# Kernel tuning notes

Hardware: AMD Instinct MI355X
Metric: run time of the kernel (lower is better)

The kernel has to match this reference:

```python
import jax, jax.numpy as jnp
import numpy as np

B, H, N, D = 1, 8, 2048, 64  # n >> d: fastmax's intended long-seq / small-head-dim regime


def setup_inputs() -> dict:
    key = jax.random.key(0)
    kq, kk, kv, kr = jax.random.split(key, 4)
    q = jax.random.normal(kq, (B, H, N, D), dtype=jnp.float32)
    k = jax.random.normal(kk, (B, H, N, D), dtype=jnp.float32)
    v = jax.random.normal(kv, (B, H, N, D), dtype=jnp.float32)
    rpe_matrix = jax.random.normal(kr, (2 * N - 1, D), dtype=jnp.float32)
    return {"q": q, "k": k, "v": v, "rpe_matrix": rpe_matrix, "mask": 1}


def reference(q, k, v, rpe_matrix, mask):
    # Fastmax: 2nd-order Taylor approximation of softmax attention,
    # weight(i,j) = 1 + s_ij + s_ij^2 / 2 where s_ij = q_i . (k_j) + q_i . rpe[i-j+n-1],
    # normalized by the row-sum, optionally causal (mask).
    b, h, n, d = q.shape
    # content scores: (b,h,n,n)
    s = jnp.einsum('bhid,bhjd->bhij', q, k)
    # RPE scores: project q onto every relative-position embedding, then gather
    # the (i,j) -> i-j+n-1 diagonal structure.  qr: (b,h,n,2n-1)
    qr = jnp.einsum('bhid,md->bhim', q, rpe_matrix)
    i = jnp.arange(n)[:, None]
    j = jnp.arange(n)[None, :]
    rel = i - j + (n - 1)  # (n,n) in [0, 2n-2]
    s = s + jnp.take_along_axis(qr, rel[None, None], axis=-1)
    # Taylor-2 exp approximation
    w = 1.0 + s + 0.5 * s * s
    if mask:  # causal
        w = jnp.where(j <= i, w, 0.0)
    denom = jnp.sum(w, axis=-1, keepdims=True)  # (b,h,n,1)
    out = jnp.einsum('bhij,bhjd->bhid', w, v) / denom
    return out
```

## Files before the change

### kernel.cpp

```cpp
#include <hip/hip_runtime.h>
#include <hip/hip_bf16.h>

#define HH 8
#define NN 2048
#define DD 64

typedef __attribute__((ext_vector_type(8))) short bf16x8;
typedef __attribute__((ext_vector_type(4))) float f32x4;
typedef __attribute__((ext_vector_type(8))) unsigned short u16x8;
typedef unsigned short ushort_t;

static __device__ __forceinline__ unsigned short f2bf(float x) {
    union { float f; unsigned u; } un; un.f = x;
    unsigned r = un.u + 0x7FFFu + ((un.u >> 16) & 1u);
    return (unsigned short)(r >> 16);
}
static __device__ __forceinline__ float bf2f(unsigned short u) {
    union { unsigned u; float f; } un; un.u = ((unsigned)u) << 16;
    return un.f;
}

#define OFF_Q  0u
#define OFF_K  2097152u
#define OFF_VT 4194304u
#define OFF_R  6291456u
#define OFF_P  6815744u
#define WS_NEED 11272192u

#define NQ4 262144
#define NR4 65520
#define CVT_BLOCKS 2305
__global__ void pre_kernel(const float* __restrict__ q, const float* __restrict__ k,
                           const float* __restrict__ r, const float* __restrict__ v,
                           ushort_t* __restrict__ ws) {
    __shared__ __align__(16) ushort_t T[64][72];
    if (blockIdx.x < CVT_BLOCKS) {
        int idx = blockIdx.x * 256 + threadIdx.x;
        const float* src; ushort_t* dst; int off;
        if (idx < NQ4) { src = q; dst = (ushort_t*)((char*)ws + OFF_Q); off = idx; }
        else if (idx < 2 * NQ4) { src = k; dst = (ushort_t*)((char*)ws + OFF_K); off = idx - NQ4; }
        else if (idx < 2 * NQ4 + NR4) { src = r; dst = (ushort_t*)((char*)ws + OFF_R); off = idx - 2 * NQ4; }
        else return;
        float4 f = *(const float4*)&src[4 * (size_t)off];
        ushort4 u; u.x = f2bf(f.x); u.y = f2bf(f.y); u.z = f2bf(f.z); u.w = f2bf(f.w);
        *(ushort4*)&dst[4 * (size_t)off] = u;
    } else {
        ushort_t* vt = (ushort_t*)((char*)ws + OFF_VT);
        const int bb = blockIdx.x - CVT_BLOCKS;
        const int h = bb >> 5;
        const int n0 = (bb & 31) * 64;
        const int tid = threadIdx.x;
        const float* vh = v + (size_t)h * NN * DD;
        #pragma unroll
        for (int p = 0; p < 4; ++p) {
            int c = tid + 256 * p; int rr = c >> 4, dc = (c & 15) << 2;
            float4 f = *(const float4*)&vh[(size_t)(n0 + rr) * DD + dc];
            T[dc + 0][rr] = f2bf(f.x); T[dc + 1][rr] = f2bf(f.y);
            T[dc + 2][rr] = f2bf(f.z); T[dc + 3][rr] = f2bf(f.w);
        }
        __syncthreads();
        #pragma unroll
        for (int p = 0; p < 2; ++p) {
            int c = tid + 256 * p; int d = c >> 3, nn = (c & 7) << 3;
            *(u16x8*)&vt[((size_t)h * 64 + d) * NN + n0 + nn] = *(const u16x8*)&T[d][nn];
        }
    }
}

__global__ __launch_bounds__(256, 2)
void fastmax_main(const ushort_t* __restrict__ wsb, float* __restrict__ outg,
                  float* __restrict__ wsPart)
{
    __shared__ __align__(16) ushort_t Ks[64][72];
    __shared__ __align__(16) ushort_t Bs[96][72];
    __shared__ __align__(16) ushort_t Vts[64][72];
    __shared__ __align__(16) float    Ts[4][16][50];
    __shared__ __align__(16) ushort_t Ws[4][16][40];
    __shared__ __align__(16) float    Epi[32][68];

    const ushort_t* qb  = (const ushort_t*)((const char*)wsb + OFF_Q);
    const ushort_t* kb  = (const ushort_t*)((const char*)wsb + OFF_K);
    const ushort_t* vtb = (const ushort_t*)((const char*)wsb + OFF_VT);
    const ushort_t* rb  = (const ushort_t*)((const char*)wsb + OFF_R);

    const int tid = threadIdx.x;
    const int w   = tid >> 6;
    const int l   = tid & 63;
    const int lq  = l >> 4;
    const int ln  = l & 15;
    const int rt  = w & 1;
    const int ch  = w >> 1;

    const int sb     = blockIdx.x & 1;
    const int stream = blockIdx.x >> 1;
    const int head   = stream & 7;
    const int p      = stream >> 3;
    const int tileA  = 63 - p;
    const int njtA   = (tileA >> 1) + 1;
    const int tileB  = p;
    const int njtB   = (tileB >> 1) + 1;

    const ushort_t* qh  = qb  + (size_t)head * NN * DD;
    const ushort_t* kh  = kb  + (size_t)head * NN * DD;
    const ushort_t* vth = vtb + (size_t)head * DD * NN;
    float*          oh  = outg + (size_t)head * NN * DD;

    const int sw = 16 * rt - 32 * ch + 32;

    #pragma unroll 1
    for (int tsel = 0; tsel < 2; ++tsel) {
        if (tsel == 1 && sb == 0) break;
        const int tile = tsel ? tileB : tileA;
        const int jlo  = tsel ? 0 : (sb ? 17 : 0);
        const int jhi  = tsel ? njtB : (sb ? njtA : 17);
        const int i0   = tile * 32;

        bf16x8 qf0 = *(const bf16x8*)&qh[(size_t)(i0 + 16 * rt + ln) * DD +  0 + 8 * lq];
        bf16x8 qf1 = *(const bf16x8*)&qh[(size_t)(i0 + 16 * rt + ln) * DD + 32 + 8 * lq];

        f32x4 acc0 = {0,0,0,0}, acc1 = {0,0,0,0}, acc2 = {0,0,0,0}, acc3 = {0,0,0,0};
        float denv0 = 0.f, denv1 = 0.f, denv2 = 0.f, denv3 = 0.f;

        for (int jt = jlo; jt < jhi; ++jt) {
            const int j0 = jt * 64;
            __syncthreads();

            #pragma unroll
            for (int p2 = 0; p2 < 2; ++p2) {
                int c = tid + 256 * p2; int r = c >> 3, dc = (c & 7) << 3;
                *(u16x8*)&Ks[r][dc] = *(const u16x8*)&kh[(size_t)(j0 + r) * DD + dc];
            }
            const int relbase = i0 - j0 + 1984;
            #pragma unroll
            for (int p2 = 0; p2 < 3; ++p2) {
                int c = tid + 256 * p2; int r = c >> 3, dc = (c & 7) << 3;
                int row = relbase + r; if (row > 4094) row = 4094;
                *(u16x8*)&Bs[r][dc] = *(const u16x8*)&rb[(size_t)row * DD + dc];
            }
            #pragma unroll
            for (int p2 = 0; p2 < 2; ++p2) {
                int c = tid + 256 * p2; int d = c >> 3, nc = (c & 7) << 3;
                *(u16x8*)&Vts[d][nc] = *(const u16x8*)&vth[(size_t)d * NN + j0 + nc];
            }
            __syncthreads();

            f32x4 s0 = {0,0,0,0}, s1 = {0,0,0,0};
            {
                bf16x8 b00 = *(const bf16x8*)&Ks[32 * ch      + ln][ 0 + 8 * lq];
                bf16x8 b01 = *(const bf16x8*)&Ks[32 * ch      + ln][32 + 8 * lq];
                bf16x8 b10 = *(const bf16x8*)&Ks[32 * ch + 16 + ln][ 0 + 8 * lq];
                bf16x8 b11 = *(const bf16x8*)&Ks[32 * ch + 16 + ln][32 + 8 * lq];
                s0 = __builtin_amdgcn_mfma_f32_16x16x32_bf16(qf0, b00, s0, 0, 0, 0);
                s0 = __builtin_amdgcn_mfma_f32_16x16x32_bf16(qf1, b01, s0, 0, 0, 0);
                s1 = __builtin_amdgcn_mfma_f32_16x16x32_bf16(qf0, b10, s1, 0, 0, 0);
                s1 = __builtin_amdgcn_mfma_f32_16x16x32_bf16(qf1, b11, s1, 0, 0, 0);
            }

            #pragma unroll
            for (int bt = 0; bt < 3; ++bt) {
                f32x4 t = {0,0,0,0};
                bf16x8 b0 = *(const bf16x8*)&Bs[sw + 16 * bt + ln][ 0 + 8 * lq];
                bf16x8 b1 = *(const bf16x8*)&Bs[sw + 16 * bt + ln][32 + 8 * lq];
                t = __builtin_amdgcn_mfma_f32_16x16x32_bf16(qf0, b0, t, 0, 0, 0);
                t = __builtin_amdgcn_mfma_f32_16x16x32_bf16(qf1, b1, t, 0, 0, 0);
                #pragma unroll
                for (int e = 0; e < 4; ++e)
                    Ts[w][4 * lq + e][16 * bt + ln] = t[e];
            }

            #pragma unroll
            for (int ct = 0; ct < 2; ++ct) {
                f32x4 sv = ct ? s1 : s0;
                #pragma unroll
                for (int e = 0; e < 4; ++e) {
                    int rp = 4 * lq + e;
                    int cp = 16 * ct + ln;
                    int bw = rp - cp + 31;
                    float s = sv[e] + Ts[w][rp][bw];
                    float wv = 1.0f + s + 0.5f * s * s;
                    if (j0 + 32 * ch + cp > i0 + 16 * rt + rp) wv = 0.0f;
                    ushort_t wb = f2bf(wv);
                    Ws[w][rp][cp] = wb;
                    float wr = bf2f(wb);
                    if (e == 0) denv0 += wr; else if (e == 1) denv1 += wr;
                    else if (e == 2) denv2 += wr; else denv3 += wr;
                }
            }

            {
                bf16x8 af = *(const bf16x8*)&Ws[w][ln][8 * lq];
                bf16x8 b;
                b = *(const bf16x8*)&Vts[ 0 + ln][32 * ch + 8 * lq];
                acc0 = __builtin_amdgcn_mfma_f32_16x16x32_bf16(af, b, acc0, 0, 0, 0);
                b = *(const bf16x8*)&Vts[16 + ln][32 * ch + 8 * lq];
                acc1 = __builtin_amdgcn_mfma_f32_16x16x32_bf16(af, b, acc1, 0, 0, 0);
                b = *(const bf16x8*)&Vts[32 + ln][32 * ch + 8 * lq];
                acc2 = __builtin_amdgcn_mfma_f32_16x16x32_bf16(af, b, acc2, 0, 0, 0);
                b = *(const bf16x8*)&Vts[48 + ln][32 * ch + 8 * lq];
                acc3 = __builtin_amdgcn_mfma_f32_16x16x32_bf16(af, b, acc3, 0, 0, 0);
            }
        }

        #pragma unroll
        for (int off = 1; off <= 8; off <<= 1) {
            denv0 += __shfl_xor(denv0, off);
            denv1 += __shfl_xor(denv1, off);
            denv2 += __shfl_xor(denv2, off);
            denv3 += __shfl_xor(denv3, off);
        }

        __syncthreads();
        if (ch == 0) {
            #pragma unroll
            for (int e = 0; e < 4; ++e) {
                int r = 16 * rt + 4 * lq + e;
                f32x4 a = (e == 0) ? acc0 : acc0;
                (void)a;
                Epi[r][ 0 + ln] = acc0[e];
                Epi[r][16 + ln] = acc1[e];
                Epi[r][32 + ln] = acc2[e];
                Epi[r][48 + ln] = acc3[e];
            }
            if (ln == 0) {
                Epi[16 * rt + 4 * lq + 0][64] = denv0;
                Epi[16 * rt + 4 * lq + 1][64] = denv1;
                Epi[16 * rt + 4 * lq + 2][64] = denv2;
                Epi[16 * rt + 4 * lq + 3][64] = denv3;
            }
        }
        __syncthreads();
        if (ch == 1) {
            #pragma unroll
            for (int e = 0; e < 4; ++e) {
                int r = 16 * rt + 4 * lq + e;
                Epi[r][ 0 + ln] += acc0[e];
                Epi[r][16 + ln] += acc1[e];
                Epi[r][32 + ln] += acc2[e];
                Epi[r][48 + ln] += acc3[e];
            }
            if (ln == 0) {
                Epi[16 * rt + 4 * lq + 0][64] += denv0;
                Epi[16 * rt + 4 * lq + 1][64] += denv1;
                Epi[16 * rt + 4 * lq + 2][64] += denv2;
                Epi[16 * rt + 4 * lq + 3][64] += denv3;
            }
        }
        __syncthreads();
        if (tsel == 0) {
            float* dst = wsPart + ((size_t)(head * 32 + p) * 2 + sb) * (32 * 68);
            for (int idx = tid; idx < 32 * 68; idx += 256) dst[idx] = (&Epi[0][0])[idx];
        } else {
            #pragma unroll
            for (int e2 = 0; e2 < 8; ++e2) {
                int idx = tid + 256 * e2;
                int r = idx >> 6, d = idx & 63;
                oh[(size_t)(i0 + r) * DD + d] = Epi[r][d] / Epi[r][64];
            }
        }
    }
}

__global__ void combine_kernel(const float* __restrict__ wsPart, float* __restrict__ outg) {
    const int blk = blockIdx.x;
    const int head = blk >> 5;
    const int p = blk & 31;
    const int tileA = 63 - p;
    const float* p0 = wsPart + (size_t)blk * 2 * (32 * 68);
    const float* p1 = p0 + 32 * 68;
    float* oh = outg + (size_t)head * NN * DD;
    #pragma unroll
    for (int e2 = 0; e2 < 8; ++e2) {
        int idx = threadIdx.x + 256 * e2;
        int r = idx >> 6, d = idx & 63;
        float num = p0[r * 68 + d] + p1[r * 68 + d];
        float den = p0[r * 68 + 64] + p1[r * 68 + 64];
        oh[(size_t)(tileA * 32 + r) * DD + d] = num / den;
    }
}

__global__ __launch_bounds__(256, 2)
void fastmax_fallback(const float* __restrict__ qg0, const float* __restrict__ kg0,
                      const float* __restrict__ vg0, const float* __restrict__ rg,
                      float* __restrict__ outg)
{
    __shared__ __align__(16) ushort_t Qs[32][72];
    __shared__ __align__(16) ushort_t Ks2[64][72];
    __shared__ __align__(16) ushort_t Bs2[96][72];
    __shared__ __align__(16) ushort_t Vts2[96][72];
    __shared__ __align__(16) float    Tsf[32][97];
    __shared__ __align__(16) ushort_t Wsf[32][72];
    __shared__ float denomLds[32];

    const int tid = threadIdx.x;
    const int w = tid >> 6, l = tid & 63, lq = l >> 4, ln = l & 15;
    const int head = blockIdx.x & 7, ib = blockIdx.x >> 3;
    const int it = 63 - ib, i0 = it * 32, njt = (it >> 1) + 1;
    const float* qg = qg0 + (size_t)head * NN * DD;
    const float* kg = kg0 + (size_t)head * NN * DD;
    const float* vg = vg0 + (size_t)head * NN * DD;
    float* og = outg + (size_t)head * NN * DD;
    {
        #pragma unroll
        for (int p = 0; p < 2; ++p) {
            int c = tid + 256 * p; int r = c >> 4, dc = (c & 15) << 2;
            float4 f = *(const float4*)&qg[(size_t)(i0 + r) * DD + dc];
            ushort4 u; u.x = f2bf(f.x); u.y = f2bf(f.y); u.z = f2bf(f.z); u.w = f2bf(f.w);
            *(ushort4*)&Qs[r][dc] = u;
        }
        for (int idx = tid; idx < 32 * 72; idx += 256) {
            int rr = idx / 72, cc = idx - rr * 72;
            Vts2[64 + rr][cc] = (rr == 0) ? (ushort_t)0x3F80 : (ushort_t)0;
        }
    }
    f32x4 a0 = {0,0,0,0}, a1 = {0,0,0,0}, a2 = {0,0,0,0};
    const int pr = w & 1, rt = w & 1, cp = w >> 1;
    for (int jt = 0; jt < njt; ++jt) {
        const int j0 = jt * 64;
        __syncthreads();
        #pragma unroll
        for (int p = 0; p < 4; ++p) {
            int c = tid + 256 * p; int r = c >> 4, dc = (c & 15) << 2;
            float4 f = *(const float4*)&kg[(size_t)(j0 + r) * DD + dc];
            ushort4 u; u.x = f2bf(f.x); u.y = f2bf(f.y); u.z = f2bf(f.z); u.w = f2bf(f.w);
            *(ushort4*)&Ks2[r][dc] = u;
        }
        const int relbase = i0 - j0 + 1984;
        #pragma unroll
        for (int p = 0; p < 6; ++p) {
            int c = tid + 256 * p; int r = c >> 4, dc = (c & 15) << 2;
            int row = relbase + r; if (row > 4094) row = 4094;
            float4 f = *(const float4*)&rg[(size_t)row * DD + dc];
            ushort4 u; u.x = f2bf(f.x); u.y = f2bf(f.y); u.z = f2bf(f.z); u.w = f2bf(f.w);
            *(ushort4*)&Bs2[r][dc] = u;
        }
        #pragma unroll
        for (int p = 0; p < 4; ++p) {
            int c = tid + 256 * p; int r = c >> 4, dc = (c & 15) << 2;
            float4 f = *(const float4*)&vg[(size_t)(j0 + r) * DD + dc];
            Vts2[dc + 0][r] = f2bf(f.x); Vts2[dc + 1][r] = f2bf(f.y);
            Vts2[dc + 2][r] = f2bf(f.z); Vts2[dc + 3][r] = f2bf(f.w);
        }
        __syncthreads();
        f32x4 s0 = {0,0,0,0}, s1 = {0,0,0,0};
        #pragma unroll
        for (int ks = 0; ks < 2; ++ks) {
            bf16x8 a = *(const bf16x8*)&Qs[16 * rt + ln][32 * ks + 8 * lq];
            bf16x8 b0 = *(const bf16x8*)&Ks2[32 * cp + ln][32 * ks + 8 * lq];
            bf16x8 b1 = *(const bf16x8*)&Ks2[32 * cp + 16 + ln][32 * ks + 8 * lq];
            s0 = __builtin_amdgcn_mfma_f32_16x16x32_bf16(a, b0, s0, 0, 0, 0);
            s1 = __builtin_amdgcn_mfma_f32_16x16x32_bf16(a, b1, s1, 0, 0, 0);
        }
        #pragma unroll
        for (int kk = 0; kk < 3; ++kk) {
            int bt = (w >> 1) + 2 * kk;
            f32x4 t = {0,0,0,0};
            #pragma unroll
            for (int ks = 0; ks < 2; ++ks) {
                bf16x8 a = *(const bf16x8*)&Qs[16 * rt + ln][32 * ks + 8 * lq];
                bf16x8 b = *(const bf16x8*)&Bs2[16 * bt + ln][32 * ks + 8 * lq];
                t = __builtin_amdgcn_mfma_f32_16x16x32_bf16(a, b, t, 0, 0, 0);
            }
            #pragma unroll
            for (int e = 0; e < 4; ++e) Tsf[16 * rt + 4 * lq + e][16 * bt + ln] = t[e];
        }
        __syncthreads();
        #pragma unroll
        for (int ct2 = 0; ct2 < 2; ++ct2) {
            f32x4 sv = ct2 ? s1 : s0;
            int c_loc = 32 * cp + 16 * ct2 + ln, j = j0 + c_loc;
            #pragma unroll
            for (int e = 0; e < 4; ++e) {
                int r_loc = 16 * rt + 4 * lq + e, i = i0 + r_loc;
                float s = sv[e] + Tsf[r_loc][r_loc - c_loc + 63];
                float wv = 1.0f + s + 0.5f * s * s;
                if (j > i) wv = 0.0f;
                Wsf[r_loc][c_loc] = f2bf(wv);
            }
        }
        __syncthreads();
        {
            bf16x8 af0 = *(const bf16x8*)&Wsf[16 * pr + ln][ 0 + 8 * lq];
            bf16x8 af1 = *(const bf16x8*)&Wsf[16 * pr + ln][32 + 8 * lq];
            int pn0 = w >> 1; bf16x8 b;
            b = *(const bf16x8*)&Vts2[16 * (pn0 + 0) + ln][ 0 + 8 * lq];
            a0 = __builtin_amdgcn_mfma_f32_16x16x32_bf16(af0, b, a0, 0, 0, 0);
            b = *(const bf16x8*)&Vts2[16 * (pn0 + 0) + ln][32 + 8 * lq];
            a0 = __builtin_amdgcn_mfma_f32_16x16x32_bf16(af1, b, a0, 0, 0, 0);
            b = *(const bf16x8*)&Vts2[16 * (pn0 + 2) + ln][ 0 + 8 * lq];
            a1 = __builtin_amdgcn_mfma_f32_16x16x32_bf16(af0, b, a1, 0, 0, 0);
            b = *(const bf16x8*)&Vts2[16 * (pn0 + 2) + ln][32 + 8 * lq];
            a1 = __builtin_amdgcn_mfma_f32_16x16x32_bf16(af1, b, a1, 0, 0, 0);
            b = *(const bf16x8*)&Vts2[16 * (pn0 + 4) + ln][ 0 + 8 * lq];
            a2 = __builtin_amdgcn_mfma_f32_16x16x32_bf16(af0, b, a2, 0, 0, 0);
            b = *(const bf16x8*)&Vts2[16 * (pn0 + 4) + ln][32 + 8 * lq];
            a2 = __builtin_amdgcn_mfma_f32_16x16x32_bf16(af1, b, a2, 0, 0, 0);
        }
    }
    if (w < 2 && ln == 0) {
        #pragma unroll
        for (int e = 0; e < 4; ++e) denomLds[16 * pr + 4 * lq + e] = a2[e];
    }
    __syncthreads();
    #pragma unroll
    for (int k = 0; k < 2; ++k) {
        int pn = (w >> 1) + 2 * k;
        f32x4 acc = k ? a1 : a0;
        #pragma unroll
        for (int e = 0; e < 4; ++e) {
            int r_loc = 16 * pr + 4 * lq + e;
            og[(size_t)(i0 + r_loc) * DD + 16 * pn + ln] = acc[e] / denomLds[r_loc];
        }
    }
}

extern "C" void kernel_launch(void* const* d_in, const int* in_sizes, int n_in,
                              void* d_out, int out_size, void* d_ws, size_t ws_size,
                              hipStream_t stream) {
    const float* q   = (const float*)d_in[0];
    const float* k   = (const float*)d_in[1];
    const float* v   = (const float*)d_in[2];
    const float* rpe = (const float*)d_in[3];
    float* out = (float*)d_out;

    if (ws_size >= WS_NEED) {
        ushort_t* wsb = (ushort_t*)d_ws;
        float* wsPart = (float*)((char*)d_ws + OFF_P);
        hipLaunchKernelGGL(pre_kernel, dim3(CVT_BLOCKS + 256), dim3(256), 0, stream,
                           q, k, rpe, v, wsb);
        hipLaunchKernelGGL(fastmax_main, dim3(512), dim3(256), 0, stream,
                           wsb, out, wsPart);
        hipLaunchKernelGGL(combine_kernel, dim3(256), dim3(256), 0, stream, wsPart, out);
    } else {
        hipLaunchKernelGGL(fastmax_fallback, dim3(512), dim3(256), 0, stream,
                           q, k, v, rpe, out);
    }
}
```

Measured before the change: 106.1 us.

## Double-buffer K/RPE/V tiles with register prefetch and store RPE scores as bf16

The K, RPE-band and V^T tiles are now double-buffered in LDS. The next tile's global loads are issued into registers before the compute on the current tile, which lets one barrier per iteration be dropped and hides global latency behind the MFMAs. To pay for the extra LDS, the per-wave RPE score scratch is stored as bf16 and aliased with the epilogue buffer in a shared union. The bf16 scratch adds rounding to the RPE score term, and the larger register and LDS footprint may lower occupancy under the 256x2 launch bound.

```diff
diff --git a/kernel.cpp b/kernel.cpp
--- a/kernel.cpp
+++ b/kernel.cpp
@@ -71,17 +71,18 @@
 void fastmax_main(const ushort_t* __restrict__ wsb, float* __restrict__ outg,
                   float* __restrict__ wsPart)
 {
-    __shared__ __align__(16) ushort_t Ks[64][72];
-    __shared__ __align__(16) ushort_t Bs[96][72];
-    __shared__ __align__(16) ushort_t Vts[64][72];
-    __shared__ __align__(16) float    Ts[4][16][50];
-    __shared__ __align__(16) ushort_t Ws[4][16][40];
-    __shared__ __align__(16) float    Epi[32][68];
+    __shared__ __align__(16) ushort_t Ks[2][64][72];
+    __shared__ __align__(16) ushort_t Bs[2][96][72];
+    __shared__ __align__(16) ushort_t Vts[2][64][72];
+    __shared__ __align__(16) unsigned char U[11776];
+    ushort_t* TsP = (ushort_t*)U;
+    ushort_t* WsP = (ushort_t*)(U + 6656);
+    float*    Epi = (float*)U;
 
     const ushort_t* qb  = (const ushort_t*)((const char*)wsb + OFF_Q);
     const ushort_t* kb  = (const ushort_t*)((const char*)wsb + OFF_K);
     const ushort_t* vtb = (const ushort_t*)((const char*)wsb + OFF_VT);
-    const ushort_t* rb  = (const ushort_t*)((const char*)wsb + OFF_R);
+    const ushort_t* rb_ = (const ushort_t*)((const char*)wsb + OFF_R);
 
     const int tid = threadIdx.x;
     const int w   = tid >> 6;
@@ -107,6 +108,11 @@
 
     const int sw = 16 * rt - 32 * ch + 32;
 
+    u16x8 rk0, rk1, rbA, rbB, rbC, rv0, rv1;
+    const int c0r = tid >> 3,         c0d = (tid & 7) << 3;
+    const int c1r = (tid + 256) >> 3, c1d = ((tid + 256) & 7) << 3;
+    const int c2r = (tid + 512) >> 3, c2d = ((tid + 512) & 7) << 3;
+
     #pragma unroll 1
     for (int tsel = 0; tsel < 2; ++tsel) {
         if (tsel == 1 && sb == 0) break;
@@ -121,35 +127,56 @@
         f32x4 acc0 = {0,0,0,0}, acc1 = {0,0,0,0}, acc2 = {0,0,0,0}, acc3 = {0,0,0,0};
         float denv0 = 0.f, denv1 = 0.f, denv2 = 0.f, denv3 = 0.f;
 
+        {
+            const int j0 = jlo * 64;
+            const int relbase = i0 - j0 + 1984;
+            rk0 = *(const u16x8*)&kh[(size_t)(j0 + c0r) * DD + c0d];
+            rk1 = *(const u16x8*)&kh[(size_t)(j0 + c1r) * DD + c1d];
+            int r0 = relbase + c0r; if (r0 > 4094) r0 = 4094;
+            int r1 = relbase + c1r; if (r1 > 4094) r1 = 4094;
+            int r2 = relbase + c2r; if (r2 > 4094) r2 = 4094;
+            rbA = *(const u16x8*)&rb_[(size_t)r0 * DD + c0d];
+            rbB = *(const u16x8*)&rb_[(size_t)r1 * DD + c1d];
+            rbC = *(const u16x8*)&rb_[(size_t)r2 * DD + c2d];
+            rv0 = *(const u16x8*)&vth[(size_t)c0r * NN + j0 + c0d];
+            rv1 = *(const u16x8*)&vth[(size_t)c1r * NN + j0 + c1d];
+        }
+
+        int buf = 0;
         for (int jt = jlo; jt < jhi; ++jt) {
             const int j0 = jt * 64;
-            __syncthreads();
-
-            #pragma unroll
-            for (int p2 = 0; p2 < 2; ++p2) {
-                int c = tid + 256 * p2; int r = c >> 3, dc = (c & 7) << 3;
-                *(u16x8*)&Ks[r][dc] = *(const u16x8*)&kh[(size_t)(j0 + r) * DD + dc];
-            }
-            const int relbase = i0 - j0 + 1984;
-            #pragma unroll
-            for (int p2 = 0; p2 < 3; ++p2) {
-                int c = tid + 256 * p2; int r = c >> 3, dc = (c & 7) << 3;
-                int row = relbase + r; if (row > 4094) row = 4094;
-                *(u16x8*)&Bs[r][dc] = *(const u16x8*)&rb[(size_t)row * DD + dc];
-            }
-            #pragma unroll
-            for (int p2 = 0; p2 < 2; ++p2) {
-                int c = tid + 256 * p2; int d = c >> 3, nc = (c & 7) << 3;
-                *(u16x8*)&Vts[d][nc] = *(const u16x8*)&vth[(size_t)d * NN + j0 + nc];
-            }
+
+            *(u16x8*)&Ks[buf][c0r][c0d] = rk0;
+            *(u16x8*)&Ks[buf][c1r][c1d] = rk1;
+            *(u16x8*)&Bs[buf][c0r][c0d] = rbA;
+            *(u16x8*)&Bs[buf][c1r][c1d] = rbB;
+            *(u16x8*)&Bs[buf][c2r][c2d] = rbC;
+            *(u16x8*)&Vts[buf][c0r][c0d] = rv0;
+            *(u16x8*)&Vts[buf][c1r][c1d] = rv1;
+
+            if (jt + 1 < jhi) {
+                const int jn = j0 + 64;
+                const int relbase = i0 - jn + 1984;
+                rk0 = *(const u16x8*)&kh[(size_t)(jn + c0r) * DD + c0d];
+                rk1 = *(const u16x8*)&kh[(size_t)(jn + c1r) * DD + c1d];
+                int r0 = relbase + c0r; if (r0 > 4094) r0 = 4094;
+                int r1 = relbase + c1r; if (r1 > 4094) r1 = 4094;
+                int r2 = relbase + c2r; if (r2 > 4094) r2 = 4094;
+                rbA = *(const u16x8*)&rb_[(size_t)r0 * DD + c0d];
+                rbB = *(const u16x8*)&rb_[(size_t)r1 * DD + c1d];
+                rbC = *(const u16x8*)&rb_[(size_t)r2 * DD + c2d];
+                rv0 = *(const u16x8*)&vth[(size_t)c0r * NN + jn + c0d];
+                rv1 = *(const u16x8*)&vth[(size_t)c1r * NN + jn + c1d];
+            }
+
             __syncthreads();
 
             f32x4 s0 = {0,0,0,0}, s1 = {0,0,0,0};
             {
-                bf16x8 b00 = *(const bf16x8*)&Ks[32 * ch      + ln][ 0 + 8 * lq];
-                bf16x8 b01 = *(const bf16x8*)&Ks[32 * ch      + ln][32 + 8 * lq];
-                bf16x8 b10 = *(const bf16x8*)&Ks[32 * ch + 16 + ln][ 0 + 8 * lq];
-                bf16x8 b11 = *(const bf16x8*)&Ks[32 * ch + 16 + ln][32 + 8 * lq];
+                bf16x8 b00 = *(const bf16x8*)&Ks[buf][32 * ch      + ln][ 0 + 8 * lq];
+                bf16x8 b01 = *(const bf16x8*)&Ks[buf][32 * ch      + ln][32 + 8 * lq];
+                bf16x8 b10 = *(const bf16x8*)&Ks[buf][32 * ch + 16 + ln][ 0 + 8 * lq];
+                bf16x8 b11 = *(const bf16x8*)&Ks[buf][32 * ch + 16 + ln][32 + 8 * lq];
                 s0 = __builtin_amdgcn_mfma_f32_16x16x32_bf16(qf0, b00, s0, 0, 0, 0);
                 s0 = __builtin_amdgcn_mfma_f32_16x16x32_bf16(qf1, b01, s0, 0, 0, 0);
                 s1 = __builtin_amdgcn_mfma_f32_16x16x32_bf16(qf0, b10, s1, 0, 0, 0);
@@ -159,13 +186,13 @@
             #pragma unroll
             for (int bt = 0; bt < 3; ++bt) {
                 f32x4 t = {0,0,0,0};
-                bf16x8 b0 = *(const bf16x8*)&Bs[sw + 16 * bt + ln][ 0 + 8 * lq];
-                bf16x8 b1 = *(const bf16x8*)&Bs[sw + 16 * bt + ln][32 + 8 * lq];
+                bf16x8 b0 = *(const bf16x8*)&Bs[buf][sw + 16 * bt + ln][ 0 + 8 * lq];
+                bf16x8 b1 = *(const bf16x8*)&Bs[buf][sw + 16 * bt + ln][32 + 8 * lq];
                 t = __builtin_amdgcn_mfma_f32_16x16x32_bf16(qf0, b0, t, 0, 0, 0);
                 t = __builtin_amdgcn_mfma_f32_16x16x32_bf16(qf1, b1, t, 0, 0, 0);
                 #pragma unroll
                 for (int e = 0; e < 4; ++e)
-                    Ts[w][4 * lq + e][16 * bt + ln] = t[e];
+                    TsP[(w * 16 + 4 * lq + e) * 52 + 16 * bt + ln] = f2bf(t[e]);
             }
 
             #pragma unroll
@@ -176,11 +203,11 @@
                     int rp = 4 * lq + e;
                     int cp = 16 * ct + ln;
                     int bw = rp - cp + 31;
-                    float s = sv[e] + Ts[w][rp][bw];
+                    float s = sv[e] + bf2f(TsP[(w * 16 + rp) * 52 + bw]);
                     float wv = 1.0f + s + 0.5f * s * s;
                     if (j0 + 32 * ch + cp > i0 + 16 * rt + rp) wv = 0.0f;
                     ushort_t wb = f2bf(wv);
-                    Ws[w][rp][cp] = wb;
+                    WsP[(w * 16 + rp) * 40 + cp] = wb;
                     float wr = bf2f(wb);
                     if (e == 0) denv0 += wr; else if (e == 1) denv1 += wr;
                     else if (e == 2) denv2 += wr; else denv3 += wr;
@@ -188,17 +215,18 @@
             }
 
             {
-                bf16x8 af = *(const bf16x8*)&Ws[w][ln][8 * lq];
+                bf16x8 af = *(const bf16x8*)&WsP[(w * 16 + ln) * 40 + 8 * lq];
                 bf16x8 b;
-                b = *(const bf16x8*)&Vts[ 0 + ln][32 * ch + 8 * lq];
+                b = *(const bf16x8*)&Vts[buf][ 0 + ln][32 * ch + 8 * lq];
                 acc0 = __builtin_amdgcn_mfma_f32_16x16x32_bf16(af, b, acc0, 0, 0, 0);
-                b = *(const bf16x8*)&Vts[16 + ln][32 * ch + 8 * lq];
+                b = *(const bf16x8*)&Vts[buf][16 + ln][32 * ch + 8 * lq];
                 acc1 = __builtin_amdgcn_mfma_f32_16x16x32_bf16(af, b, acc1, 0, 0, 0);
-                b = *(const bf16x8*)&Vts[32 + ln][32 * ch + 8 * lq];
+                b = *(const bf16x8*)&Vts[buf][32 + ln][32 * ch + 8 * lq];
                 acc2 = __builtin_amdgcn_mfma_f32_16x16x32_bf16(af, b, acc2, 0, 0, 0);
-                b = *(const bf16x8*)&Vts[48 + ln][32 * ch + 8 * lq];
+                b = *(const bf16x8*)&Vts[buf][48 + ln][32 * ch + 8 * lq];
                 acc3 = __builtin_amdgcn_mfma_f32_16x16x32_bf16(af, b, acc3, 0, 0, 0);
             }
+            buf ^= 1;
         }
 
         #pragma unroll
@@ -214,18 +242,16 @@
             #pragma unroll
             for (int e = 0; e < 4; ++e) {
                 int r = 16 * rt + 4 * lq + e;
-                f32x4 a = (e == 0) ? acc0 : acc0;
-                (void)a;
-                Epi[r][ 0 + ln] = acc0[e];
-                Epi[r][16 + ln] = acc1[e];
-                Epi[r][32 + ln] = acc2[e];
-                Epi[r][48 + ln] = acc3[e];
+                Epi[r * 68 +  0 + ln] = acc0[e];
+                Epi[r * 68 + 16 + ln] = acc1[e];
+                Epi[r * 68 + 32 + ln] = acc2[e];
+                Epi[r * 68 + 48 + ln] = acc3[e];
             }
             if (ln == 0) {
-                Epi[16 * rt + 4 * lq + 0][64] = denv0;
-                Epi[16 * rt + 4 * lq + 1][64] = denv1;
-                Epi[16 * rt + 4 * lq + 2][64] = denv2;
-                Epi[16 * rt + 4 * lq + 3][64] = denv3;
+                Epi[(16 * rt + 4 * lq + 0) * 68 + 64] = denv0;
+                Epi[(16 * rt + 4 * lq + 1) * 68 + 64] = denv1;
+                Epi[(16 * rt + 4 * lq + 2) * 68 + 64] = denv2;
+                Epi[(16 * rt + 4 * lq + 3) * 68 + 64] = denv3;
             }
         }
         __syncthreads();
@@ -233,28 +259,28 @@
             #pragma unroll
             for (int e = 0; e < 4; ++e) {
                 int r = 16 * rt + 4 * lq + e;
-                Epi[r][ 0 + ln] += acc0[e];
-                Epi[r][16 + ln] += acc1[e];
-                Epi[r][32 + ln] += acc2[e];
-                Epi[r][48 + ln] += acc3[e];
+                Epi[r * 68 +  0 + ln] += acc0[e];
+                Epi[r * 68 + 16 + ln] += acc1[e];
+                Epi[r * 68 + 32 + ln] += acc2[e];
+                Epi[r * 68 + 48 + ln] += acc3[e];
             }
             if (ln == 0) {
-                Epi[16 * rt + 4 * lq + 0][64] += denv0;
-                Epi[16 * rt + 4 * lq + 1][64] += denv1;
-                Epi[16 * rt + 4 * lq + 2][64] += denv2;
-                Epi[16 * rt + 4 * lq + 3][64] += denv3;
+                Epi[(16 * rt + 4 * lq + 0) * 68 + 64] += denv0;
+                Epi[(16 * rt + 4 * lq + 1) * 68 + 64] += denv1;
+                Epi[(16 * rt + 4 * lq + 2) * 68 + 64] += denv2;
+                Epi[(16 * rt + 4 * lq + 3) * 68 + 64] += denv3;
             }
         }
         __syncthreads();
         if (tsel == 0) {
             float* dst = wsPart + ((size_t)(head * 32 + p) * 2 + sb) * (32 * 68);
-            for (int idx = tid; idx < 32 * 68; idx += 256) dst[idx] = (&Epi[0][0])[idx];
+            for (int idx = tid; idx < 32 * 68; idx += 256) dst[idx] = Epi[idx];
         } else {
             #pragma unroll
             for (int e2 = 0; e2 < 8; ++e2) {
                 int idx = tid + 256 * e2;
                 int r = idx >> 6, d = idx & 63;
-                oh[(size_t)(i0 + r) * DD + d] = Epi[r][d] / Epi[r][64];
+                oh[(size_t)(i0 + r) * DD + d] = Epi[r * 68 + d] / Epi[r * 68 + 64];
             }
         }
     }
```

Result: no change. 104.7 us (-1.4%).
